# Kernel optimization log

Measured on AMD Instinct MI355X. Metric: run time of the kernel, lower is better.

Reference implementation:

```python
import jax, jax.numpy as jnp
import numpy as np

N_KW, N_RT = 100000, 20000
D, H, O = 128, 128, 128
E_A, E_B, E_C = 1600000, 1600000, 320000


def setup_inputs() -> dict:
    key = jax.random.key(0)
    ks = jax.random.split(key, 32)
    inp = {
        "x_kw": jax.random.normal(ks[0], (N_KW, D), jnp.float32),
        "x_rt": jax.random.normal(ks[1], (N_RT, D), jnp.float32),
        "src_a": jax.random.randint(ks[2], (E_A,), 0, N_RT),
        "dst_a": jax.random.randint(ks[3], (E_A,), 0, N_KW),
        "src_b": jax.random.randint(ks[4], (E_B,), 0, N_KW),
        "dst_b": jax.random.randint(ks[5], (E_B,), 0, N_KW),
        "src_c": jax.random.randint(ks[6], (E_C,), 0, N_RT),
        "dst_c": jax.random.randint(ks[7], (E_C,), 0, N_RT),
    }
    # SAGEConv params per relation per layer: W_l (neighbor), b_l, W_r (root, no bias)
    i = 8
    dims = {1: (D, H), 2: (H, O)}
    for layer in (1, 2):
        din, dout = dims[layer]
        for rel in ("a", "b", "c"):
            inp[f"Wl{layer}{rel}"] = jax.random.normal(ks[i], (din, dout), jnp.float32) * 0.05; i += 1
            inp[f"bl{layer}{rel}"] = jnp.zeros((dout,), jnp.float32)
            inp[f"Wr{layer}{rel}"] = jax.random.normal(ks[i], (din, dout), jnp.float32) * 0.05; i += 1
    return inp


def _sage(x_src, x_dst, src, dst, Wl, bl, Wr):
    # PyG SAGEConv (mean aggr): lin_l(mean_j x_src[j]) + lin_r(x_dst)
    n = x_dst.shape[0]
    s = jax.ops.segment_sum(x_src[src], dst, num_segments=n)      # [n, din]
    cnt = jax.ops.segment_sum(jnp.ones_like(dst, dtype=x_src.dtype), dst, num_segments=n)
    mean = s / jnp.maximum(cnt, 1.0)[:, None]
    return mean @ Wl + bl + x_dst @ Wr


def reference(x_kw, x_rt, src_a, dst_a, src_b, dst_b, src_c, dst_c,
              Wl1a, bl1a, Wr1a, Wl1b, bl1b, Wr1b, Wl1c, bl1c, Wr1c,
              Wl2a, bl2a, Wr2a, Wl2b, bl2b, Wr2b, Wl2c, bl2c, Wr2c):
    # layer 1 (HeteroConv aggr='sum' over relations sharing a dst type)
    kw1 = (_sage(x_rt, x_kw, src_a, dst_a, Wl1a, bl1a, Wr1a)
           + _sage(x_kw, x_kw, src_b, dst_b, Wl1b, bl1b, Wr1b))
    rt1 = _sage(x_rt, x_rt, src_c, dst_c, Wl1c, bl1c, Wr1c)
    kw1 = jax.nn.relu(kw1)
    rt1 = jax.nn.relu(rt1)
    # layer 2
    kw2 = (_sage(rt1, kw1, src_a, dst_a, Wl2a, bl2a, Wr2a)
           + _sage(kw1, kw1, src_b, dst_b, Wl2b, bl2b, Wr2b))
    rt2 = _sage(rt1, rt1, src_c, dst_c, Wl2c, bl2c, Wr2c)
    return kw2, rt2
```

## Files before the change

kernel.cpp:

```cpp
#include <hip/hip_runtime.h>

typedef __attribute__((ext_vector_type(8))) short bf16x8;
typedef __attribute__((ext_vector_type(4))) float f32x4;
typedef __attribute__((ext_vector_type(2))) float f32x2;

static __device__ __forceinline__ unsigned short f2bf(float f) {
    unsigned int u = __float_as_uint(f);
    u += 0x7fffu + ((u >> 16) & 1u);
    return (unsigned short)(u >> 16);
}
static __device__ __forceinline__ float bf2f(unsigned short h) {
    return __uint_as_float(((unsigned int)h) << 16);
}

#define BSH 6
#define BUCKET 64
#define NBMAX 1600
#define CHSH 13


struct Rel {
    const int* src; const int* dst; int E; int nb; int Ndst;
    int hblk0, hnblk;
    int sblk0, snblk;
    int oblk0;
    int shift;
    int* bcnt; int* boff; int* bcur;
    unsigned* pairs; unsigned* ssrc; int* goff; float* invd;
};
struct Rels { Rel r[3]; };

struct PrepArgs {
    const float* W[10];
    const float* Wa[10];
    const float* b1a; const float* b1b; const float* b2a; const float* b2b;
};


__global__ void prep_hist_k(PrepArgs pa, unsigned short* __restrict__ Wt,
                            float* __restrict__ bc1, float* __restrict__ bc2,
                            Rels R, int prepBlocks) {
    int bid = blockIdx.x;
    if (bid < prepBlocks) {
        if (bid < 640) {
            int slot = bid >> 6;
            int i = ((bid & 63) << 8) + threadIdx.x;
            float v = pa.W[slot][i];
            const float* w2 = pa.Wa[slot];
            if (w2) v += w2[i];
            int k = i >> 7, n = i & 127;
            Wt[slot * 16384 + n * 128 + k] = f2bf(v);
        } else {
            int t = threadIdx.x;
            if (t < 128) bc1[t] = pa.b1a[t] + pa.b1b[t];
            else bc2[t - 128] = pa.b2a[t - 128] + pa.b2b[t - 128];
        }
        return;
    }
    int hb = bid - prepBlocks;
    const Rel* r;
    if (hb < R.r[1].hblk0) r = &R.r[0];
    else if (hb < R.r[2].hblk0) r = &R.r[1];
    else r = &R.r[2];
    __shared__ int h[NBMAX];
    for (int i = threadIdx.x; i < r->nb; i += 256) h[i] = 0;
    __syncthreads();
    for (int e = (hb - r->hblk0) * 256 + threadIdx.x; e < r->E; e += r->hnblk * 256)
        atomicAdd(&h[r->dst[e] >> BSH], 1);
    __syncthreads();
    for (int i = threadIdx.x; i < r->nb; i += 256)
        if (h[i]) atomicAdd(&r->bcnt[i], h[i]);
}


__global__ void bscan3_k(Rels R) {
    const Rel* r = &R.r[blockIdx.x];
    __shared__ int s[1024];
    int t = threadIdx.x;
    int nb = r->nb;
    int e0 = 2 * t, e1 = 2 * t + 1;
    int v0 = (e0 < nb) ? r->bcnt[e0] : 0;
    int v1 = (e1 < nb) ? r->bcnt[e1] : 0;
    s[t] = v0 + v1;
    __syncthreads();
    for (int o = 1; o < 1024; o <<= 1) {
        int x = (t >= o) ? s[t - o] : 0;
        __syncthreads();
        s[t] += x;
        __syncthreads();
    }
    int P = s[t] - (v0 + v1);
    if (e0 <= nb) { r->boff[e0] = P; if (e0 < nb) r->bcur[e0] = 0; }
    if (e1 <= nb) { r->boff[e1] = P + v0; if (e1 < nb) r->bcur[e1] = 0; }
}

__global__ __launch_bounds__(256) void bscatter3_k(Rels R) {
    const Rel* r;
    int bid = blockIdx.x;
    if (bid < R.r[1].sblk0) r = &R.r[0];
    else if (bid < R.r[2].sblk0) r = &R.r[1];
    else r = &R.r[2];
    __shared__ int h[NBMAX];
    __shared__ int base[NBMAX];
    int t = threadIdx.x;
    int nb = r->nb, E = r->E;
    for (int i = t; i < nb; i += 256) h[i] = 0;
    __syncthreads();
    int e0 = (bid - r->sblk0) * 8192;
    for (int i = 0; i < 32; i++) {
        int e = e0 + i * 256 + t;
        if (e < E) atomicAdd(&h[r->dst[e] >> BSH], 1);
    }
    __syncthreads();
    for (int i = t; i < nb; i += 256) {
        int c = h[i];
        base[i] = c ? (r->boff[i] + atomicAdd(&r->bcur[i], c)) : 0;
    }
    __syncthreads();
    for (int i = t; i < nb; i += 256) h[i] = 0;
    __syncthreads();
    for (int i = 0; i < 32; i++) {
        int e = e0 + i * 256 + t;
        if (e < E) {
            int d = r->dst[e];
            int b = d >> BSH;
            int pos = base[b] + atomicAdd(&h[b], 1);
            r->pairs[pos] = ((unsigned)(d & (BUCKET - 1)) << 17) | (unsigned)r->src[e];
        }
    }
}

static __device__ void sortb_body(const Rels& R, int bid) {
    const Rel* r;
    if (bid < R.r[1].oblk0) r = &R.r[0];
    else if (bid < R.r[2].oblk0) r = &R.r[1];
    else r = &R.r[2];
    int b = bid - r->oblk0;
    __shared__ int cnt[1024];
    __shared__ int sc[256];
    int t = threadIdx.x;
    for (int i = t; i < 1024; i += 256) cnt[i] = 0;
    __syncthreads();
    int j0 = r->boff[b], j1 = r->boff[b + 1];
    for (int j = j0 + t; j < j1; j += 256) {
        unsigned p = r->pairs[j];
        int d = (p >> 17) & 63;
        int ch = (int)((p & 0x1ffffu) >> CHSH); if (ch > 15) ch = 15;
        int bin = ((d & 7) << 7) | ((d >> 3) << 4) | ch;
        atomicAdd(&cnt[bin], 1);
    }
    __syncthreads();
    if (t < 64) {
        int b0 = ((t & 7) << 7) | ((t >> 3) << 4);
        int c = 0;
#pragma unroll
        for (int i = 0; i < 16; i++) c += cnt[b0 + i];
        int dd = (b << BSH) + t;
        if (dd < r->Ndst) r->invd[dd] = 1.f / (float)(c > 0 ? c : 1);
    }
    int c0 = cnt[4 * t], c1 = cnt[4 * t + 1], c2 = cnt[4 * t + 2], c3 = cnt[4 * t + 3];
    int tot = c0 + c1 + c2 + c3;
    sc[t] = tot;
    __syncthreads();
    for (int o = 1; o < 256; o <<= 1) {
        int x = (t >= o) ? sc[t - o] : 0;
        __syncthreads();
        sc[t] += x;
        __syncthreads();
    }
    int base = j0 + sc[t] - tot;
    if ((t & 3) == 0) r->goff[b * 64 + (t >> 2)] = base;
    cnt[4 * t] = base;
    cnt[4 * t + 1] = base + c0;
    cnt[4 * t + 2] = base + c0 + c1;
    cnt[4 * t + 3] = base + c0 + c1 + c2;
    if (t == 0 && b == r->nb - 1) r->goff[r->nb * 64] = r->E;
    __syncthreads();
    int shift = r->shift;
    for (int j = j0 + t; j < j1; j += 256) {
        unsigned p = r->pairs[j];
        int d = (p >> 17) & 63;
        int ch = (int)((p & 0x1ffffu) >> CHSH); if (ch > 15) ch = 15;
        int bin = ((d & 7) << 7) | ((d >> 3) << 4) | ch;
        int pos = atomicAdd(&cnt[bin], 1);
        r->ssrc[pos] = (p & 0x1ffffu) << shift;
    }
}


struct GemmJobs {
    const void* Akw; int Nkw;
    const unsigned short* Wk1; const float* bk; unsigned short* Zkw;
    const unsigned short* Wk2; unsigned char* Ckw8;
    const void* Art; int Nrt;
    const unsigned short* Wr1; const float* br; unsigned short* Zrt;
    const unsigned short* Wr2; unsigned short* Crt2;
    const unsigned short* Wr3; unsigned short* Crt3;
    int kwBlocks;
};

template <int AF32>
static __device__ void gemm_body(const GemmJobs& G, int bid) {
    bool iskw = bid < G.kwBlocks;
    const void* A = iskw ? G.Akw : G.Art;
    int N = iskw ? G.Nkw : G.Nrt;
    int lane = threadIdx.x & 63;
    int r16 = lane & 15, g = lane >> 4;
    int row0 = (iskw ? bid : bid - G.kwBlocks) * 64 + (threadIdx.x >> 6) * 16;
    int arow = row0 + r16;
    int arow_c = arow < N ? arow : N - 1;

    bf16x8 af[4];
    if (AF32) {
        const float* Af = (const float*)A + (size_t)arow_c * 128 + g * 8;
#pragma unroll
        for (int kc = 0; kc < 4; kc++) {
            float4 u0 = *(const float4*)(Af + kc * 32);
            float4 u1 = *(const float4*)(Af + kc * 32 + 4);
            bf16x8 rr;
            rr[0] = (short)f2bf(u0.x); rr[1] = (short)f2bf(u0.y);
            rr[2] = (short)f2bf(u0.z); rr[3] = (short)f2bf(u0.w);
            rr[4] = (short)f2bf(u1.x); rr[5] = (short)f2bf(u1.y);
            rr[6] = (short)f2bf(u1.z); rr[7] = (short)f2bf(u1.w);
            af[kc] = rr;
        }
    } else {
        const bf16x8* Ar = (const bf16x8*)((const unsigned short*)A + (size_t)arow_c * 128);
#pragma unroll
        for (int kc = 0; kc < 4; kc++) af[kc] = Ar[kc * 4 + g];
    }

    if (iskw) {
        f32x4 acc1[8], acc2[8];
#pragma unroll
        for (int ct = 0; ct < 8; ct++) { f32x4 z = {0.f,0.f,0.f,0.f}; acc1[ct] = z; acc2[ct] = z; }
#pragma unroll
        for (int kc = 0; kc < 4; kc++) {
#pragma unroll
            for (int ct = 0; ct < 8; ct++) {
                int wo = ((ct * 16 + r16) << 7) + kc * 32 + g * 8;
                bf16x8 b1 = *(const bf16x8*)(G.Wk1 + wo);
                acc1[ct] = __builtin_amdgcn_mfma_f32_16x16x32_bf16(af[kc], b1, acc1[ct], 0, 0, 0);
                bf16x8 b2 = *(const bf16x8*)(G.Wk2 + wo);
                acc2[ct] = __builtin_amdgcn_mfma_f32_16x16x32_bf16(af[kc], b2, acc2[ct], 0, 0, 0);
            }
        }
#pragma unroll
        for (int ct = 0; ct < 8; ct++) {
            int col = ct * 16 + r16;
            float bb = G.bk[col];
#pragma unroll
            for (int j = 0; j < 4; j++) {
                int r = row0 + g * 4 + j;
                if (r < N) {
                    G.Zkw[(size_t)r * 128 + col] = f2bf(acc1[ct][j] + bb);
                    float v2 = acc2[ct][j];
                    int pk = __builtin_amdgcn_cvt_pk_fp8_f32(v2, v2, 0, false);
                    G.Ckw8[(size_t)r * 128 + col] = (unsigned char)(pk & 0xff);
                }
            }
        }
    } else {
        f32x4 acc1[8], acc2[8], acc3[8];
#pragma unroll
        for (int ct = 0; ct < 8; ct++) {
            f32x4 z = {0.f,0.f,0.f,0.f}; acc1[ct] = z; acc2[ct] = z; acc3[ct] = z;
        }
#pragma unroll
        for (int kc = 0; kc < 4; kc++) {
#pragma unroll
            for (int ct = 0; ct < 8; ct++) {
                int wo = ((ct * 16 + r16) << 7) + kc * 32 + g * 8;
                bf16x8 b1 = *(const bf16x8*)(G.Wr1 + wo);
                acc1[ct] = __builtin_amdgcn_mfma_f32_16x16x32_bf16(af[kc], b1, acc1[ct], 0, 0, 0);
                bf16x8 b2 = *(const bf16x8*)(G.Wr2 + wo);
                acc2[ct] = __builtin_amdgcn_mfma_f32_16x16x32_bf16(af[kc], b2, acc2[ct], 0, 0, 0);
                bf16x8 b3 = *(const bf16x8*)(G.Wr3 + wo);
                acc3[ct] = __builtin_amdgcn_mfma_f32_16x16x32_bf16(af[kc], b3, acc3[ct], 0, 0, 0);
            }
        }
#pragma unroll
        for (int ct = 0; ct < 8; ct++) {
            int col = ct * 16 + r16;
            float bb = G.br[col];
#pragma unroll
            for (int j = 0; j < 4; j++) {
                int r = row0 + g * 4 + j;
                if (r < N) {
                    G.Zrt[(size_t)r * 128 + col] = f2bf(acc1[ct][j] + bb);
                    G.Crt2[(size_t)r * 128 + col] = f2bf(acc2[ct][j]);
                    G.Crt3[(size_t)r * 128 + col] = f2bf(acc3[ct][j]);
                }
            }
        }
    }
}

__global__ __launch_bounds__(256) void gemm_sort_k(GemmJobs G, Rels R, int gemmBlocks) {
    if ((int)blockIdx.x < gemmBlocks) gemm_body<1>(G, blockIdx.x);
    else sortb_body(R, blockIdx.x - gemmBlocks);
}

__global__ __launch_bounds__(256) void gemm_l2_k(GemmJobs G) {
    gemm_body<0>(G, blockIdx.x);
}

template <int FMT>
static __device__ __forceinline__ void agg_rel(float* acc, int b, int w, int lane,
                                               int dst0,
                                               const unsigned* __restrict__ sp,
                                               const int* __restrict__ goff,
                                               const float* __restrict__ invd,
                                               const char* __restrict__ Ybase) {
    int g = lane >> 4, q = lane & 15;
    int lb = FMT ? (q << 3) : (q << 4);
    int idx0 = (0 + g) << 2, idx1 = (4 + g) << 2, idx2 = (8 + g) << 2, idx3 = (12 + g) << 2;
    int loc0 = (((2 * g) & 3) << 5) + 2 * q + (g >> 1);
    int loc1 = (((2 * g + 1) & 3) << 5) + 2 * q + (g >> 1);
#pragma unroll 1
    for (int r = 0; r < 8; r++) {
        int gi = b * 64 + w * 8 + r;
        int jg0 = goff[gi], jg1 = goff[gi + 1];
        if (jg0 >= jg1) continue;
        int d = (r << 3) | w;
        f32x2 a01 = {0.f, 0.f}, a23 = {0.f, 0.f}, a45 = {0.f, 0.f}, a67 = {0.f, 0.f};
#pragma unroll 1
        for (int jb = jg0; jb < jg1; jb += 32) {
            int ji = jb + (lane & 31);
            ji = ji < jg1 ? ji : jg1 - 1;
            int spv = (int)sp[ji];
            if (jb + 32 <= jg1) {
#pragma unroll
                for (int hb = 0; hb < 2; hb++) {
                    int hofs = hb << 6;
                    unsigned o0 = (unsigned)__builtin_amdgcn_ds_bpermute(idx0 + hofs, spv);
                    unsigned o1 = (unsigned)__builtin_amdgcn_ds_bpermute(idx1 + hofs, spv);
                    unsigned o2 = (unsigned)__builtin_amdgcn_ds_bpermute(idx2 + hofs, spv);
                    unsigned o3 = (unsigned)__builtin_amdgcn_ds_bpermute(idx3 + hofs, spv);
                    if (FMT == 0) {
                        uint4 v0 = *(const uint4*)(Ybase + o0 + lb);
                        uint4 v1 = *(const uint4*)(Ybase + o1 + lb);
                        uint4 v2 = *(const uint4*)(Ybase + o2 + lb);
                        uint4 v3 = *(const uint4*)(Ybase + o3 + lb);
#pragma unroll
                        for (int k = 0; k < 4; k++) {
                            uint4 v = k == 0 ? v0 : k == 1 ? v1 : k == 2 ? v2 : v3;
                            f32x2 x0 = { __uint_as_float(v.x << 16), __uint_as_float(v.x & 0xffff0000u) };
                            f32x2 x1 = { __uint_as_float(v.y << 16), __uint_as_float(v.y & 0xffff0000u) };
                            f32x2 x2 = { __uint_as_float(v.z << 16), __uint_as_float(v.z & 0xffff0000u) };
                            f32x2 x3 = { __uint_as_float(v.w << 16), __uint_as_float(v.w & 0xffff0000u) };
                            a01 += x0; a23 += x1; a45 += x2; a67 += x3;
                        }
                    } else {
                        uint2 v0 = *(const uint2*)(Ybase + o0 + lb);
                        uint2 v1 = *(const uint2*)(Ybase + o1 + lb);
                        uint2 v2 = *(const uint2*)(Ybase + o2 + lb);
                        uint2 v3 = *(const uint2*)(Ybase + o3 + lb);
#pragma unroll
                        for (int k = 0; k < 4; k++) {
                            uint2 v = k == 0 ? v0 : k == 1 ? v1 : k == 2 ? v2 : v3;
                            auto l0 = __builtin_amdgcn_cvt_pk_f32_fp8(v.x, false);
                            auto h0 = __builtin_amdgcn_cvt_pk_f32_fp8(v.x, true);
                            auto l1 = __builtin_amdgcn_cvt_pk_f32_fp8(v.y, false);
                            auto h1 = __builtin_amdgcn_cvt_pk_f32_fp8(v.y, true);
                            a01[0] += l0[0]; a01[1] += l0[1];
                            a23[0] += h0[0]; a23[1] += h0[1];
                            a45[0] += l1[0]; a45[1] += l1[1];
                            a67[0] += h1[0]; a67[1] += h1[1];
                        }
                    }
                }
            } else {
#pragma unroll
                for (int hb = 0; hb < 2; hb++) {
                    int ebase = jb + (hb << 4) + g;
                    if (ebase >= jg1 && g == 0) {}
                    if (jb + (hb << 4) >= jg1) break;
                    int hofs = hb << 6;
                    unsigned o0 = (unsigned)__builtin_amdgcn_ds_bpermute(idx0 + hofs, spv);
                    unsigned o1 = (unsigned)__builtin_amdgcn_ds_bpermute(idx1 + hofs, spv);
                    unsigned o2 = (unsigned)__builtin_amdgcn_ds_bpermute(idx2 + hofs, spv);
                    unsigned o3 = (unsigned)__builtin_amdgcn_ds_bpermute(idx3 + hofs, spv);
#pragma unroll
                    for (int k = 0; k < 4; k++) {
                        unsigned ok = k == 0 ? o0 : k == 1 ? o1 : k == 2 ? o2 : o3;
                        bool live = (jb + (hb << 4) + 4 * k + g) < jg1;
                        if (FMT == 0) {
                            uint4 v = *(const uint4*)(Ybase + ok + lb);
                            unsigned vx = live ? v.x : 0u, vy = live ? v.y : 0u;
                            unsigned vz = live ? v.z : 0u, vw = live ? v.w : 0u;
                            f32x2 x0 = { __uint_as_float(vx << 16), __uint_as_float(vx & 0xffff0000u) };
                            f32x2 x1 = { __uint_as_float(vy << 16), __uint_as_float(vy & 0xffff0000u) };
                            f32x2 x2 = { __uint_as_float(vz << 16), __uint_as_float(vz & 0xffff0000u) };
                            f32x2 x3 = { __uint_as_float(vw << 16), __uint_as_float(vw & 0xffff0000u) };
                            a01 += x0; a23 += x1; a45 += x2; a67 += x3;
                        } else {
                            uint2 v = *(const uint2*)(Ybase + ok + lb);
                            unsigned vx = live ? v.x : 0u, vy = live ? v.y : 0u;
                            auto l0 = __builtin_amdgcn_cvt_pk_f32_fp8(vx, false);
                            auto h0 = __builtin_amdgcn_cvt_pk_f32_fp8(vx, true);
                            auto l1 = __builtin_amdgcn_cvt_pk_f32_fp8(vy, false);
                            auto h1 = __builtin_amdgcn_cvt_pk_f32_fp8(vy, true);
                            a01[0] += l0[0]; a01[1] += l0[1];
                            a23[0] += h0[0]; a23[1] += h0[1];
                            a45[0] += l1[0]; a45[1] += l1[1];
                            a67[0] += h1[0]; a67[1] += h1[1];
                        }
                    }
                }
            }
        }
        float s0 = a01[0], s1 = a01[1], s2 = a23[0], s3 = a23[1];
        float s4 = a45[0], s5 = a45[1], s6 = a67[0], s7 = a67[1];
        s0 += __shfl_xor(s0, 16); s0 += __shfl_xor(s0, 32);
        s1 += __shfl_xor(s1, 16); s1 += __shfl_xor(s1, 32);
        s2 += __shfl_xor(s2, 16); s2 += __shfl_xor(s2, 32);
        s3 += __shfl_xor(s3, 16); s3 += __shfl_xor(s3, 32);
        s4 += __shfl_xor(s4, 16); s4 += __shfl_xor(s4, 32);
        s5 += __shfl_xor(s5, 16); s5 += __shfl_xor(s5, 32);
        s6 += __shfl_xor(s6, 16); s6 += __shfl_xor(s6, 32);
        s7 += __shfl_xor(s7, 16); s7 += __shfl_xor(s7, 32);
        float w0 = g == 0 ? s0 : g == 1 ? s2 : g == 2 ? s4 : s6;
        float w1 = g == 0 ? s1 : g == 1 ? s3 : g == 2 ? s5 : s7;
        float inv = invd[dst0 + d];
        int ba = d * 128;
        acc[ba + loc0] += w0 * inv;
        acc[ba + loc1] += w1 * inv;
    }
}

struct AggJob {
    const unsigned short* Zin; int Ndst;
    const unsigned* sp0; const int* goff0; const float* invd0; const void* Y0; int fmt0;
    const unsigned* sp1; const int* goff1; const float* invd1; const void* Y1; int fmt1;
    int nrel;
    float* OutF; unsigned short* OutB;
};

template <int RELU, int OUTBF16>
__global__ __launch_bounds__(512) void bagg2_k(AggJob JK, AggJob JR, int kwBlocks) {
    __shared__ float acc[BUCKET * 128];
    bool iskw = blockIdx.x < (unsigned)kwBlocks;
    AggJob J = iskw ? JK : JR;
    int b = iskw ? blockIdx.x : blockIdx.x - kwBlocks;
    int t = threadIdx.x;
    int dst0 = b << BSH;
    int nrow = J.Ndst - dst0; if (nrow > BUCKET) nrow = BUCKET;

    for (int c = t; c < BUCKET * 32; c += 512) {
        int r = c >> 5, m = c & 31;
        float z0 = 0.f, z1 = 0.f, z2 = 0.f, z3 = 0.f;
        if (r < nrow) {
            ushort4 z = *(const ushort4*)(J.Zin + (size_t)(dst0 + r) * 128 + (m << 2));
            z0 = bf2f(z.x); z1 = bf2f(z.y); z2 = bf2f(z.z); z3 = bf2f(z.w);
        }
        acc[r * 128 + m] = z0;
        acc[r * 128 + 32 + m] = z1;
        acc[r * 128 + 64 + m] = z2;
        acc[r * 128 + 96 + m] = z3;
    }
    __syncthreads();

    int w = t >> 6, lane = t & 63;
    if (J.fmt0 == 0) agg_rel<0>(acc, b, w, lane, dst0, J.sp0, J.goff0, J.invd0, (const char*)J.Y0);
    else agg_rel<1>(acc, b, w, lane, dst0, J.sp0, J.goff0, J.invd0, (const char*)J.Y0);
    if (J.nrel == 2) {
        if (J.fmt1 == 0) agg_rel<0>(acc, b, w, lane, dst0, J.sp1, J.goff1, J.invd1, (const char*)J.Y1);
        else agg_rel<1>(acc, b, w, lane, dst0, J.sp1, J.goff1, J.invd1, (const char*)J.Y1);
    }
    __syncthreads();
    for (int c = t; c < BUCKET * 32; c += 512) {
        int r = c >> 5, m = c & 31;
        if (r < nrow) {
            float x0 = acc[r * 128 + m];
            float x1 = acc[r * 128 + 32 + m];
            float x2 = acc[r * 128 + 64 + m];
            float x3 = acc[r * 128 + 96 + m];
            if (RELU) {
                x0 = fmaxf(x0, 0.f); x1 = fmaxf(x1, 0.f);
                x2 = fmaxf(x2, 0.f); x3 = fmaxf(x3, 0.f);
            }
            size_t o = (size_t)(dst0 + r) * 128 + (m << 2);
            if (OUTBF16) {
                ushort4 ov;
                ov.x = f2bf(x0); ov.y = f2bf(x1); ov.z = f2bf(x2); ov.w = f2bf(x3);
                *(ushort4*)(J.OutB + o) = ov;
            } else {
                *(float4*)(J.OutF + o) = make_float4(x0, x1, x2, x3);
            }
        }
    }
}


static inline size_t align256(size_t x) { return (x + 255) & ~size_t(255); }

extern "C" void kernel_launch(void* const* d_in, const int* in_sizes, int n_in,
                              void* d_out, int out_size, void* d_ws, size_t ws_size,
                              hipStream_t stream) {
    const float* x_kw = (const float*)d_in[0];
    const float* x_rt = (const float*)d_in[1];
    const int* src_a = (const int*)d_in[2];
    const int* dst_a = (const int*)d_in[3];
    const int* src_b = (const int*)d_in[4];
    const int* dst_b = (const int*)d_in[5];
    const int* src_c = (const int*)d_in[6];
    const int* dst_c = (const int*)d_in[7];
    const float *Wl1a = (const float*)d_in[8],  *bl1a = (const float*)d_in[9],  *Wr1a = (const float*)d_in[10];
    const float *Wl1b = (const float*)d_in[11], *bl1b = (const float*)d_in[12], *Wr1b = (const float*)d_in[13];
    const float *Wl1c = (const float*)d_in[14], *bl1c = (const float*)d_in[15], *Wr1c = (const float*)d_in[16];
    const float *Wl2a = (const float*)d_in[17], *bl2a = (const float*)d_in[18], *Wr2a = (const float*)d_in[19];
    const float *Wl2b = (const float*)d_in[20], *bl2b = (const float*)d_in[21], *Wr2b = (const float*)d_in[22];
    const float *Wl2c = (const float*)d_in[23], *bl2c = (const float*)d_in[24], *Wr2c = (const float*)d_in[25];

    const int NKW = in_sizes[0] / 128;
    const int NRT = in_sizes[1] / 128;
    const int EA = in_sizes[2], EB = in_sizes[4], EC = in_sizes[6];
    const int nb_kw = (NKW + BUCKET - 1) / BUCKET;
    const int nb_rt = (NRT + BUCKET - 1) / BUCKET;

    char* ws = (char*)d_ws;
    size_t off = 0;
    auto alloc = [&](size_t bytes) -> char* {
        off = align256(off);
        char* p = ws + off;
        off += bytes;
        return p;
    };
    unsigned short* Wt = (unsigned short*)alloc(10 * 16384 * 2);
    float* bc1 = (float*)alloc(128 * 4);
    float* bc2 = (float*)alloc(128 * 4);
    int* bcnt3 = (int*)alloc(3 * NBMAX * 4);
    int* bcur3 = (int*)alloc(3 * NBMAX * 4);
    int* boff_a = (int*)alloc((NBMAX + 1) * 4);
    int* boff_b = (int*)alloc((NBMAX + 1) * 4);
    int* boff_c = (int*)alloc((NBMAX + 1) * 4);
    int* goff_a = (int*)alloc(((size_t)nb_kw * 64 + 1) * 4);
    int* goff_b = (int*)alloc(((size_t)nb_kw * 64 + 1) * 4);
    int* goff_c = (int*)alloc(((size_t)nb_rt * 64 + 1) * 4);
    float* invd_a = (float*)alloc((size_t)NKW * 4);
    float* invd_b = (float*)alloc((size_t)NKW * 4);
    float* invd_c = (float*)alloc((size_t)NRT * 4);
    unsigned* pairs_a = (unsigned*)alloc((size_t)EA * 4);
    unsigned* pairs_b = (unsigned*)alloc((size_t)EB * 4);
    unsigned* pairs_c = (unsigned*)alloc((size_t)EC * 4);
    unsigned* sp_a = (unsigned*)alloc((size_t)EA * 4);
    unsigned* sp_b = (unsigned*)alloc((size_t)EB * 4);
    unsigned* sp_c = (unsigned*)alloc((size_t)EC * 4);
    unsigned short* Ya = (unsigned short*)alloc((size_t)NRT * 128 * 2);
    unsigned char*  Yb = (unsigned char*)alloc((size_t)NKW * 128);
    unsigned short* Yc = (unsigned short*)alloc((size_t)NRT * 128 * 2);
    unsigned short* Zkw = (unsigned short*)alloc((size_t)NKW * 128 * 2);
    unsigned short* Zrt = (unsigned short*)alloc((size_t)NRT * 128 * 2);
    unsigned short* kw1_bf = (unsigned short*)alloc((size_t)NKW * 128 * 2);
    unsigned short* rt1_bf = (unsigned short*)alloc((size_t)NRT * 128 * 2);
    (void)ws_size;

    float* out_kw = (float*)d_out;
    float* out_rt = out_kw + (size_t)NKW * 128;

    Rels R;
    int hA = 128, hB = 128, hC = 64;
    int sA = (EA + 8191) / 8192, sB = (EB + 8191) / 8192, sC = (EC + 8191) / 8192;
    R.r[0] = {src_a, dst_a, EA, nb_kw, NKW, 0, hA, 0, sA, 0, 8,
              bcnt3, boff_a, bcur3, pairs_a, sp_a, goff_a, invd_a};
    R.r[1] = {src_b, dst_b, EB, nb_kw, NKW, hA, hB, sA, sB, nb_kw, 7,
              bcnt3 + NBMAX, boff_b, bcur3 + NBMAX, pairs_b, sp_b, goff_b, invd_b};
    R.r[2] = {src_c, dst_c, EC, nb_rt, NRT, hA + hB, hC, sA + sB, sC, 2 * nb_kw, 8,
              bcnt3 + 2 * NBMAX, boff_c, bcur3 + 2 * NBMAX, pairs_c, sp_c, goff_c, invd_c};

    hipMemsetAsync(bcnt3, 0, 3 * NBMAX * 4, stream);
    PrepArgs pa;
    pa.W[0] = Wr1a; pa.Wa[0] = Wr1b;
    pa.W[1] = Wl1a; pa.Wa[1] = nullptr;
    pa.W[2] = Wl1b; pa.Wa[2] = nullptr;
    pa.W[3] = Wl1c; pa.Wa[3] = nullptr;
    pa.W[4] = Wr1c; pa.Wa[4] = nullptr;
    pa.W[5] = Wr2a; pa.Wa[5] = Wr2b;
    pa.W[6] = Wl2a; pa.Wa[6] = nullptr;
    pa.W[7] = Wl2b; pa.Wa[7] = nullptr;
    pa.W[8] = Wl2c; pa.Wa[8] = nullptr;
    pa.W[9] = Wr2c; pa.Wa[9] = nullptr;
    pa.b1a = bl1a; pa.b1b = bl1b; pa.b2a = bl2a; pa.b2b = bl2b;
    prep_hist_k<<<641 + hA + hB + hC, 256, 0, stream>>>(pa, Wt, bc1, bc2, R, 641);
    unsigned short* W0 = Wt + 0 * 16384;
    unsigned short* W1 = Wt + 1 * 16384;
    unsigned short* W2 = Wt + 2 * 16384;
    unsigned short* W3 = Wt + 3 * 16384;
    unsigned short* W4 = Wt + 4 * 16384;
    unsigned short* W5 = Wt + 5 * 16384;
    unsigned short* W6 = Wt + 6 * 16384;
    unsigned short* W7 = Wt + 7 * 16384;
    unsigned short* W8 = Wt + 8 * 16384;
    unsigned short* W9 = Wt + 9 * 16384;

    bscan3_k<<<3, 1024, 0, stream>>>(R);
    bscatter3_k<<<sA + sB + sC, 256, 0, stream>>>(R);

    const int kwB = (NKW + 63) / 64, rtB = (NRT + 63) / 64;
    const int nsort = 2 * nb_kw + nb_rt;

    GemmJobs G1;
    G1.Akw = x_kw; G1.Nkw = NKW; G1.Wk1 = W0; G1.bk = bc1; G1.Zkw = Zkw; G1.Wk2 = W2; G1.Ckw8 = Yb;
    G1.Art = x_rt; G1.Nrt = NRT; G1.Wr1 = W4; G1.br = bl1c; G1.Zrt = Zrt;
    G1.Wr2 = W1; G1.Crt2 = Ya; G1.Wr3 = W3; G1.Crt3 = Yc;
    G1.kwBlocks = kwB;
    gemm_sort_k<<<kwB + rtB + nsort, 256, 0, stream>>>(G1, R, kwB + rtB);

    AggJob JK1 = {Zkw, NKW, sp_a, goff_a, invd_a, Ya, 0, sp_b, goff_b, invd_b, Yb, 1, 2,
                  nullptr, kw1_bf};
    AggJob JR1 = {Zrt, NRT, sp_c, goff_c, invd_c, Yc, 0, nullptr, nullptr, nullptr, nullptr, 0, 1,
                  nullptr, rt1_bf};
    bagg2_k<1, 1><<<nb_kw + nb_rt, 512, 0, stream>>>(JK1, JR1, nb_kw);

    GemmJobs G2;
    G2.Akw = kw1_bf; G2.Nkw = NKW; G2.Wk1 = W5; G2.bk = bc2; G2.Zkw = Zkw; G2.Wk2 = W7; G2.Ckw8 = Yb;
    G2.Art = rt1_bf; G2.Nrt = NRT; G2.Wr1 = W9; G2.br = bl2c; G2.Zrt = Zrt;
    G2.Wr2 = W6; G2.Crt2 = Ya; G2.Wr3 = W8; G2.Crt3 = Yc;
    G2.kwBlocks = kwB;
    gemm_l2_k<<<kwB + rtB, 256, 0, stream>>>(G2);

    AggJob JK2 = {Zkw, NKW, sp_a, goff_a, invd_a, Ya, 0, sp_b, goff_b, invd_b, Yb, 1, 2,
                  out_kw, nullptr};
    AggJob JR2 = {Zrt, NRT, sp_c, goff_c, invd_c, Yc, 0, nullptr, nullptr, nullptr, nullptr, 0, 1,
                  out_rt, nullptr};
    bagg2_k<0, 0><<<nb_kw + nb_rt, 512, 0, stream>>>(JK2, JR2, nb_kw);
}
```

Before: 669.8 us.

## Accumulate both relations in registers and drop LDS staging in aggregation kernel

Replaces the shared-memory accumulator in the aggregation kernel with per-row register accumulation. Both relations are summed in registers and scaled by their inverse degrees. The root term Z is added after the cross-lane reduction, and ReLU and the store are applied directly per row. Edge offsets are now read straight from global memory in 16-edge chunks instead of one coalesced 32-edge load redistributed with ds_bpermute. This removes the 32 KB LDS buffer, the block-wide syncs and the separate init and writeback passes. The trade-off is more scattered index loads and shorter chunks per iteration.

```diff
diff --git a/kernel.cpp b/kernel.cpp
--- a/kernel.cpp
+++ b/kernel.cpp
@@ -306,126 +306,78 @@
 }
 
 template <int FMT>
-static __device__ __forceinline__ void agg_rel(float* acc, int b, int w, int lane,
-                                               int dst0,
-                                               const unsigned* __restrict__ sp,
-                                               const int* __restrict__ goff,
-                                               const float* __restrict__ invd,
-                                               const char* __restrict__ Ybase) {
-    int g = lane >> 4, q = lane & 15;
-    int lb = FMT ? (q << 3) : (q << 4);
-    int idx0 = (0 + g) << 2, idx1 = (4 + g) << 2, idx2 = (8 + g) << 2, idx3 = (12 + g) << 2;
-    int loc0 = (((2 * g) & 3) << 5) + 2 * q + (g >> 1);
-    int loc1 = (((2 * g + 1) & 3) << 5) + 2 * q + (g >> 1);
+static __device__ __forceinline__ void row_accum(const unsigned* __restrict__ sp,
+                                                 int jg0, int jg1,
+                                                 const char* __restrict__ Y, int lb, int g,
+                                                 f32x2& a01, f32x2& a23,
+                                                 f32x2& a45, f32x2& a67) {
 #pragma unroll 1
-    for (int r = 0; r < 8; r++) {
-        int gi = b * 64 + w * 8 + r;
-        int jg0 = goff[gi], jg1 = goff[gi + 1];
-        if (jg0 >= jg1) continue;
-        int d = (r << 3) | w;
-        f32x2 a01 = {0.f, 0.f}, a23 = {0.f, 0.f}, a45 = {0.f, 0.f}, a67 = {0.f, 0.f};
-#pragma unroll 1
-        for (int jb = jg0; jb < jg1; jb += 32) {
-            int ji = jb + (lane & 31);
-            ji = ji < jg1 ? ji : jg1 - 1;
-            int spv = (int)sp[ji];
-            if (jb + 32 <= jg1) {
-#pragma unroll
-                for (int hb = 0; hb < 2; hb++) {
-                    int hofs = hb << 6;
-                    unsigned o0 = (unsigned)__builtin_amdgcn_ds_bpermute(idx0 + hofs, spv);
-                    unsigned o1 = (unsigned)__builtin_amdgcn_ds_bpermute(idx1 + hofs, spv);
-                    unsigned o2 = (unsigned)__builtin_amdgcn_ds_bpermute(idx2 + hofs, spv);
-                    unsigned o3 = (unsigned)__builtin_amdgcn_ds_bpermute(idx3 + hofs, spv);
-                    if (FMT == 0) {
-                        uint4 v0 = *(const uint4*)(Ybase + o0 + lb);
-                        uint4 v1 = *(const uint4*)(Ybase + o1 + lb);
-                        uint4 v2 = *(const uint4*)(Ybase + o2 + lb);
-                        uint4 v3 = *(const uint4*)(Ybase + o3 + lb);
-#pragma unroll
-                        for (int k = 0; k < 4; k++) {
-                            uint4 v = k == 0 ? v0 : k == 1 ? v1 : k == 2 ? v2 : v3;
-                            f32x2 x0 = { __uint_as_float(v.x << 16), __uint_as_float(v.x & 0xffff0000u) };
-                            f32x2 x1 = { __uint_as_float(v.y << 16), __uint_as_float(v.y & 0xffff0000u) };
-                            f32x2 x2 = { __uint_as_float(v.z << 16), __uint_as_float(v.z & 0xffff0000u) };
-                            f32x2 x3 = { __uint_as_float(v.w << 16), __uint_as_float(v.w & 0xffff0000u) };
-                            a01 += x0; a23 += x1; a45 += x2; a67 += x3;
-                        }
-                    } else {
-                        uint2 v0 = *(const uint2*)(Ybase + o0 + lb);
-                        uint2 v1 = *(const uint2*)(Ybase + o1 + lb);
-                        uint2 v2 = *(const uint2*)(Ybase + o2 + lb);
-                        uint2 v3 = *(const uint2*)(Ybase + o3 + lb);
-#pragma unroll
-                        for (int k = 0; k < 4; k++) {
-                            uint2 v = k == 0 ? v0 : k == 1 ? v1 : k == 2 ? v2 : v3;
-                            auto l0 = __builtin_amdgcn_cvt_pk_f32_fp8(v.x, false);
-                            auto h0 = __builtin_amdgcn_cvt_pk_f32_fp8(v.x, true);
-                            auto l1 = __builtin_amdgcn_cvt_pk_f32_fp8(v.y, false);
-                            auto h1 = __builtin_amdgcn_cvt_pk_f32_fp8(v.y, true);
-                            a01[0] += l0[0]; a01[1] += l0[1];
-                            a23[0] += h0[0]; a23[1] += h0[1];
-                            a45[0] += l1[0]; a45[1] += l1[1];
-                            a67[0] += h1[0]; a67[1] += h1[1];
-                        }
-                    }
+    for (int jb = jg0; jb < jg1; jb += 16) {
+        if (jb + 16 <= jg1) {
+            unsigned o0 = sp[jb + g], o1 = sp[jb + 4 + g];
+            unsigned o2 = sp[jb + 8 + g], o3 = sp[jb + 12 + g];
+            if (FMT == 0) {
+                uint4 v0 = *(const uint4*)(Y + o0 + lb);
+                uint4 v1 = *(const uint4*)(Y + o1 + lb);
+                uint4 v2 = *(const uint4*)(Y + o2 + lb);
+                uint4 v3 = *(const uint4*)(Y + o3 + lb);
+#pragma unroll
+                for (int k = 0; k < 4; k++) {
+                    uint4 v = k == 0 ? v0 : k == 1 ? v1 : k == 2 ? v2 : v3;
+                    f32x2 x0 = { __uint_as_float(v.x << 16), __uint_as_float(v.x & 0xffff0000u) };
+                    f32x2 x1 = { __uint_as_float(v.y << 16), __uint_as_float(v.y & 0xffff0000u) };
+                    f32x2 x2 = { __uint_as_float(v.z << 16), __uint_as_float(v.z & 0xffff0000u) };
+                    f32x2 x3 = { __uint_as_float(v.w << 16), __uint_as_float(v.w & 0xffff0000u) };
+                    a01 += x0; a23 += x1; a45 += x2; a67 += x3;
                 }
             } else {
-#pragma unroll
-                for (int hb = 0; hb < 2; hb++) {
-                    int ebase = jb + (hb << 4) + g;
-                    if (ebase >= jg1 && g == 0) {}
-                    if (jb + (hb << 4) >= jg1) break;
-                    int hofs = hb << 6;
-                    unsigned o0 = (unsigned)__builtin_amdgcn_ds_bpermute(idx0 + hofs, spv);
-                    unsigned o1 = (unsigned)__builtin_amdgcn_ds_bpermute(idx1 + hofs, spv);
-                    unsigned o2 = (unsigned)__builtin_amdgcn_ds_bpermute(idx2 + hofs, spv);
-                    unsigned o3 = (unsigned)__builtin_amdgcn_ds_bpermute(idx3 + hofs, spv);
-#pragma unroll
-                    for (int k = 0; k < 4; k++) {
-                        unsigned ok = k == 0 ? o0 : k == 1 ? o1 : k == 2 ? o2 : o3;
-                        bool live = (jb + (hb << 4) + 4 * k + g) < jg1;
-                        if (FMT == 0) {
-                            uint4 v = *(const uint4*)(Ybase + ok + lb);
-                            unsigned vx = live ? v.x : 0u, vy = live ? v.y : 0u;
-                            unsigned vz = live ? v.z : 0u, vw = live ? v.w : 0u;
-                            f32x2 x0 = { __uint_as_float(vx << 16), __uint_as_float(vx & 0xffff0000u) };
-                            f32x2 x1 = { __uint_as_float(vy << 16), __uint_as_float(vy & 0xffff0000u) };
-                            f32x2 x2 = { __uint_as_float(vz << 16), __uint_as_float(vz & 0xffff0000u) };
-                            f32x2 x3 = { __uint_as_float(vw << 16), __uint_as_float(vw & 0xffff0000u) };
-                            a01 += x0; a23 += x1; a45 += x2; a67 += x3;
-                        } else {
-                            uint2 v = *(const uint2*)(Ybase + ok + lb);
-                            unsigned vx = live ? v.x : 0u, vy = live ? v.y : 0u;
-                            auto l0 = __builtin_amdgcn_cvt_pk_f32_fp8(vx, false);
-                            auto h0 = __builtin_amdgcn_cvt_pk_f32_fp8(vx, true);
-                            auto l1 = __builtin_amdgcn_cvt_pk_f32_fp8(vy, false);
-                            auto h1 = __builtin_amdgcn_cvt_pk_f32_fp8(vy, true);
-                            a01[0] += l0[0]; a01[1] += l0[1];
-                            a23[0] += h0[0]; a23[1] += h0[1];
-                            a45[0] += l1[0]; a45[1] += l1[1];
-                            a67[0] += h1[0]; a67[1] += h1[1];
-                        }
-                    }
+                uint2 v0 = *(const uint2*)(Y + o0 + lb);
+                uint2 v1 = *(const uint2*)(Y + o1 + lb);
+                uint2 v2 = *(const uint2*)(Y + o2 + lb);
+                uint2 v3 = *(const uint2*)(Y + o3 + lb);
+#pragma unroll
+                for (int k = 0; k < 4; k++) {
+                    uint2 v = k == 0 ? v0 : k == 1 ? v1 : k == 2 ? v2 : v3;
+                    auto l0 = __builtin_amdgcn_cvt_pk_f32_fp8(v.x, false);
+                    auto h0 = __builtin_amdgcn_cvt_pk_f32_fp8(v.x, true);
+                    auto l1 = __builtin_amdgcn_cvt_pk_f32_fp8(v.y, false);
+                    auto h1 = __builtin_amdgcn_cvt_pk_f32_fp8(v.y, true);
+                    a01[0] += l0[0]; a01[1] += l0[1];
+                    a23[0] += h0[0]; a23[1] += h0[1];
+                    a45[0] += l1[0]; a45[1] += l1[1];
+                    a67[0] += h1[0]; a67[1] += h1[1];
                 }
             }
-        }
-        float s0 = a01[0], s1 = a01[1], s2 = a23[0], s3 = a23[1];
-        float s4 = a45[0], s5 = a45[1], s6 = a67[0], s7 = a67[1];
-        s0 += __shfl_xor(s0, 16); s0 += __shfl_xor(s0, 32);
-        s1 += __shfl_xor(s1, 16); s1 += __shfl_xor(s1, 32);
-        s2 += __shfl_xor(s2, 16); s2 += __shfl_xor(s2, 32);
-        s3 += __shfl_xor(s3, 16); s3 += __shfl_xor(s3, 32);
-        s4 += __shfl_xor(s4, 16); s4 += __shfl_xor(s4, 32);
-        s5 += __shfl_xor(s5, 16); s5 += __shfl_xor(s5, 32);
-        s6 += __shfl_xor(s6, 16); s6 += __shfl_xor(s6, 32);
-        s7 += __shfl_xor(s7, 16); s7 += __shfl_xor(s7, 32);
-        float w0 = g == 0 ? s0 : g == 1 ? s2 : g == 2 ? s4 : s6;
-        float w1 = g == 0 ? s1 : g == 1 ? s3 : g == 2 ? s5 : s7;
-        float inv = invd[dst0 + d];
-        int ba = d * 128;
-        acc[ba + loc0] += w0 * inv;
-        acc[ba + loc1] += w1 * inv;
+        } else {
+#pragma unroll
+            for (int k = 0; k < 4; k++) {
+                int e = jb + 4 * k + g;
+                int ec = e < jg1 ? e : jg1 - 1;
+                bool live = e < jg1;
+                unsigned o = sp[ec];
+                if (FMT == 0) {
+                    uint4 v = *(const uint4*)(Y + o + lb);
+                    unsigned vx = live ? v.x : 0u, vy = live ? v.y : 0u;
+                    unsigned vz = live ? v.z : 0u, vw = live ? v.w : 0u;
+                    f32x2 x0 = { __uint_as_float(vx << 16), __uint_as_float(vx & 0xffff0000u) };
+                    f32x2 x1 = { __uint_as_float(vy << 16), __uint_as_float(vy & 0xffff0000u) };
+                    f32x2 x2 = { __uint_as_float(vz << 16), __uint_as_float(vz & 0xffff0000u) };
+                    f32x2 x3 = { __uint_as_float(vw << 16), __uint_as_float(vw & 0xffff0000u) };
+                    a01 += x0; a23 += x1; a45 += x2; a67 += x3;
+                } else {
+                    uint2 v = *(const uint2*)(Y + o + lb);
+                    unsigned vx = live ? v.x : 0u, vy = live ? v.y : 0u;
+                    auto l0 = __builtin_amdgcn_cvt_pk_f32_fp8(vx, false);
+                    auto h0 = __builtin_amdgcn_cvt_pk_f32_fp8(vx, true);
+                    auto l1 = __builtin_amdgcn_cvt_pk_f32_fp8(vy, false);
+                    auto h1 = __builtin_amdgcn_cvt_pk_f32_fp8(vy, true);
+                    a01[0] += l0[0]; a01[1] += l0[1];
+                    a23[0] += h0[0]; a23[1] += h0[1];
+                    a45[0] += l1[0]; a45[1] += l1[1];
+                    a67[0] += h1[0]; a67[1] += h1[1];
+                }
+            }
+        }
     }
 }
 
@@ -438,56 +390,74 @@
 };
 
 template <int RELU, int OUTBF16>
-__global__ __launch_bounds__(512) void bagg2_k(AggJob JK, AggJob JR, int kwBlocks) {
-    __shared__ float acc[BUCKET * 128];
+__global__ __launch_bounds__(512) void bagg3_k(AggJob JK, AggJob JR, int kwBlocks) {
     bool iskw = blockIdx.x < (unsigned)kwBlocks;
     AggJob J = iskw ? JK : JR;
     int b = iskw ? blockIdx.x : blockIdx.x - kwBlocks;
+    int dst0 = b << BSH;
     int t = threadIdx.x;
-    int dst0 = b << BSH;
-    int nrow = J.Ndst - dst0; if (nrow > BUCKET) nrow = BUCKET;
-
-    for (int c = t; c < BUCKET * 32; c += 512) {
-        int r = c >> 5, m = c & 31;
-        float z0 = 0.f, z1 = 0.f, z2 = 0.f, z3 = 0.f;
-        if (r < nrow) {
-            ushort4 z = *(const ushort4*)(J.Zin + (size_t)(dst0 + r) * 128 + (m << 2));
-            z0 = bf2f(z.x); z1 = bf2f(z.y); z2 = bf2f(z.z); z3 = bf2f(z.w);
-        }
-        acc[r * 128 + m] = z0;
-        acc[r * 128 + 32 + m] = z1;
-        acc[r * 128 + 64 + m] = z2;
-        acc[r * 128 + 96 + m] = z3;
-    }
-    __syncthreads();
-
     int w = t >> 6, lane = t & 63;
-    if (J.fmt0 == 0) agg_rel<0>(acc, b, w, lane, dst0, J.sp0, J.goff0, J.invd0, (const char*)J.Y0);
-    else agg_rel<1>(acc, b, w, lane, dst0, J.sp0, J.goff0, J.invd0, (const char*)J.Y0);
-    if (J.nrel == 2) {
-        if (J.fmt1 == 0) agg_rel<0>(acc, b, w, lane, dst0, J.sp1, J.goff1, J.invd1, (const char*)J.Y1);
-        else agg_rel<1>(acc, b, w, lane, dst0, J.sp1, J.goff1, J.invd1, (const char*)J.Y1);
-    }
-    __syncthreads();
-    for (int c = t; c < BUCKET * 32; c += 512) {
-        int r = c >> 5, m = c & 31;
-        if (r < nrow) {
-            float x0 = acc[r * 128 + m];
-            float x1 = acc[r * 128 + 32 + m];
-            float x2 = acc[r * 128 + 64 + m];
-            float x3 = acc[r * 128 + 96 + m];
-            if (RELU) {
-                x0 = fmaxf(x0, 0.f); x1 = fmaxf(x1, 0.f);
-                x2 = fmaxf(x2, 0.f); x3 = fmaxf(x3, 0.f);
-            }
-            size_t o = (size_t)(dst0 + r) * 128 + (m << 2);
-            if (OUTBF16) {
-                ushort4 ov;
-                ov.x = f2bf(x0); ov.y = f2bf(x1); ov.z = f2bf(x2); ov.w = f2bf(x3);
-                *(ushort4*)(J.OutB + o) = ov;
-            } else {
-                *(float4*)(J.OutF + o) = make_float4(x0, x1, x2, x3);
-            }
+    int g = lane >> 4, q = lane & 15;
+    int lb0 = J.fmt0 ? (q << 3) : (q << 4);
+    int lb1 = J.fmt1 ? (q << 3) : (q << 4);
+
+#pragma unroll 1
+    for (int r = 0; r < 8; r++) {
+        int d = (r << 3) | w;
+        if (dst0 + d >= J.Ndst) continue;
+        int gi = b * 64 + w * 8 + r;
+        f32x2 a01 = {0.f,0.f}, a23 = {0.f,0.f}, a45 = {0.f,0.f}, a67 = {0.f,0.f};
+        {
+            int jg0 = J.goff0[gi], jg1 = J.goff0[gi + 1];
+            if (J.fmt0 == 0) row_accum<0>(J.sp0, jg0, jg1, (const char*)J.Y0, lb0, g, a01, a23, a45, a67);
+            else             row_accum<1>(J.sp0, jg0, jg1, (const char*)J.Y0, lb0, g, a01, a23, a45, a67);
+        }
+        float inv0 = J.invd0[dst0 + d];
+        float r0 = a01[0] * inv0, r1 = a01[1] * inv0;
+        float r2 = a23[0] * inv0, r3 = a23[1] * inv0;
+        float r4 = a45[0] * inv0, r5 = a45[1] * inv0;
+        float r6 = a67[0] * inv0, r7 = a67[1] * inv0;
+        if (J.nrel == 2) {
+            f32x2 b01 = {0.f,0.f}, b23 = {0.f,0.f}, b45 = {0.f,0.f}, b67 = {0.f,0.f};
+            int jg0 = J.goff1[gi], jg1 = J.goff1[gi + 1];
+            if (J.fmt1 == 0) row_accum<0>(J.sp1, jg0, jg1, (const char*)J.Y1, lb1, g, b01, b23, b45, b67);
+            else             row_accum<1>(J.sp1, jg0, jg1, (const char*)J.Y1, lb1, g, b01, b23, b45, b67);
+            float inv1 = J.invd1[dst0 + d];
+            r0 = fmaf(b01[0], inv1, r0); r1 = fmaf(b01[1], inv1, r1);
+            r2 = fmaf(b23[0], inv1, r2); r3 = fmaf(b23[1], inv1, r3);
+            r4 = fmaf(b45[0], inv1, r4); r5 = fmaf(b45[1], inv1, r5);
+            r6 = fmaf(b67[0], inv1, r6); r7 = fmaf(b67[1], inv1, r7);
+        }
+        r0 += __shfl_xor(r0, 16); r0 += __shfl_xor(r0, 32);
+        r1 += __shfl_xor(r1, 16); r1 += __shfl_xor(r1, 32);
+        r2 += __shfl_xor(r2, 16); r2 += __shfl_xor(r2, 32);
+        r3 += __shfl_xor(r3, 16); r3 += __shfl_xor(r3, 32);
+        r4 += __shfl_xor(r4, 16); r4 += __shfl_xor(r4, 32);
+        r5 += __shfl_xor(r5, 16); r5 += __shfl_xor(r5, 32);
+        r6 += __shfl_xor(r6, 16); r6 += __shfl_xor(r6, 32);
+        r7 += __shfl_xor(r7, 16); r7 += __shfl_xor(r7, 32);
+        uint4 zz = *(const uint4*)((const char*)J.Zin + (((size_t)(dst0 + d)) << 8) + (q << 4));
+        r0 += __uint_as_float(zz.x << 16); r1 += __uint_as_float(zz.x & 0xffff0000u);
+        r2 += __uint_as_float(zz.y << 16); r3 += __uint_as_float(zz.y & 0xffff0000u);
+        r4 += __uint_as_float(zz.z << 16); r5 += __uint_as_float(zz.z & 0xffff0000u);
+        r6 += __uint_as_float(zz.w << 16); r7 += __uint_as_float(zz.w & 0xffff0000u);
+        if (RELU) {
+            r0 = fmaxf(r0, 0.f); r1 = fmaxf(r1, 0.f); r2 = fmaxf(r2, 0.f); r3 = fmaxf(r3, 0.f);
+            r4 = fmaxf(r4, 0.f); r5 = fmaxf(r5, 0.f); r6 = fmaxf(r6, 0.f); r7 = fmaxf(r7, 0.f);
+        }
+        if (OUTBF16) {
+            if (g == 0) {
+                uint4 ov;
+                ov.x = (unsigned)f2bf(r0) | ((unsigned)f2bf(r1) << 16);
+                ov.y = (unsigned)f2bf(r2) | ((unsigned)f2bf(r3) << 16);
+                ov.z = (unsigned)f2bf(r4) | ((unsigned)f2bf(r5) << 16);
+                ov.w = (unsigned)f2bf(r6) | ((unsigned)f2bf(r7) << 16);
+                *(uint4*)((char*)J.OutB + (((size_t)(dst0 + d)) << 8) + (q << 4)) = ov;
+            }
+        } else {
+            float* orow = J.OutF + ((size_t)(dst0 + d) << 7) + (q << 3);
+            if (g == 0) *(float4*)orow = make_float4(r0, r1, r2, r3);
+            if (g == 1) *(float4*)(orow + 4) = make_float4(r4, r5, r6, r7);
         }
     }
 }
@@ -611,7 +581,7 @@
                   nullptr, kw1_bf};
     AggJob JR1 = {Zrt, NRT, sp_c, goff_c, invd_c, Yc, 0, nullptr, nullptr, nullptr, nullptr, 0, 1,
                   nullptr, rt1_bf};
-    bagg2_k<1, 1><<<nb_kw + nb_rt, 512, 0, stream>>>(JK1, JR1, nb_kw);
+    bagg3_k<1, 1><<<nb_kw + nb_rt, 512, 0, stream>>>(JK1, JR1, nb_kw);
 
     GemmJobs G2;
     G2.Akw = kw1_bf; G2.Nkw = NKW; G2.Wk1 = W5; G2.bk = bc2; G2.Zkw = Zkw; G2.Wk2 = W7; G2.Ckw8 = Yb;
@@ -624,5 +594,5 @@
                   out_kw, nullptr};
     AggJob JR2 = {Zrt, NRT, sp_c, goff_c, invd_c, Yc, 0, nullptr, nullptr, nullptr, nullptr, 0, 1,
                   out_rt, nullptr};
-    bagg2_k<0, 0><<<nb_kw + nb_rt, 512, 0, stream>>>(JK2, JR2, nb_kw);
-}
+    bagg3_k<0, 0><<<nb_kw + nb_rt, 512, 0, stream>>>(JK2, JR2, nb_kw);
+}
```

Result: faster. 606.6 us (-9.4%).
